# Kernel tuning notes

Hardware: AMD Instinct MI355X
Metric: run time of the kernel (lower is better)

## Reference

```python
import jax, jax.numpy as jnp
import numpy as np

B, S, D, H = 2, 2048, 1024, 16
DK = D // H

def setup_inputs() -> dict:
    key = jax.random.key(0)
    ks = jax.random.split(key, 11)
    def lin(kw, kb):
        # torch nn.Linear init scale ~ 1/sqrt(fan_in)
        s = 1.0 / np.sqrt(D)
        W = jax.random.uniform(kw, (D, D), jnp.float32, -s, s)
        b = jax.random.uniform(kb, (D,), jnp.float32, -s, s)
        return W, b
    Wq, bq = lin(ks[0], ks[1])
    Wk, bk = lin(ks[2], ks[3])
    Wv, bv = lin(ks[4], ks[5])
    Wo, bo = lin(ks[6], ks[7])
    query = jax.random.normal(ks[8], (B, S, D), jnp.float32)
    key_t = jax.random.normal(ks[9], (B, S, D), jnp.float32)
    value = jax.random.normal(ks[10], (B, S, D), jnp.float32)
    return {"query": query, "key": key_t, "value": value,
            "Wq": Wq, "bq": bq, "Wk": Wk, "bk": bk,
            "Wv": Wv, "bv": bv, "Wo": Wo, "bo": bo}

def reference(query, key, value, Wq, bq, Wk, bk, Wv, bv, Wo, bo):
    # linear projections (torch Linear: x @ W.T + b), split heads -> (B,H,S,DK)
    def proj(x, W, b):
        y = jnp.einsum('bsd,ed->bse', x, W) + b
        return y.reshape(B, -1, H, DK).transpose(0, 2, 1, 3)
    q = proj(query, Wq, bq)
    k = proj(key, Wk, bk)
    v = proj(value, Wv, bv)
    # scaled dot-product attention, full score matrix (B,H,Sq,Sk)
    scores = jnp.einsum('bhqd,bhkd->bhqk', q, k) / jnp.sqrt(jnp.float32(DK))
    attn = jax.nn.softmax(scores, axis=-1)
    ctx = jnp.einsum('bhqk,bhkd->bhqd', attn, v)
    # merge heads and output projection; dropout is identity in eval mode
    ctx = ctx.transpose(0, 2, 1, 3).reshape(B, -1, D)
    out = jnp.einsum('bsd,ed->bse', ctx, Wo) + bo
    attn_weights = attn.mean(axis=1)  # average_weights=True -> (B,Sq,Sk)
    return (out, attn_weights)
```

## Files before the change

### kernel.cpp

```cpp
#include <hip/hip_runtime.h>

#define B_ 2
#define S_ 2048
#define D_ 1024
#define H_ 16
#define DK_ 64
#define M_ (B_ * S_)

typedef __bf16 bf16;
typedef __attribute__((ext_vector_type(8))) __bf16 bf16x8;
typedef __attribute__((ext_vector_type(4))) __bf16 bf16x4;
typedef __attribute__((ext_vector_type(4))) float f32x4;

static __device__ __forceinline__ bf16x8 ld8(const bf16* p) {
    return *(const bf16x8*)p;
}

static __device__ __forceinline__ void g2l16(const void* g, void* l) {
    __builtin_amdgcn_global_load_lds(
        (const __attribute__((address_space(1))) unsigned int*)g,
        (__attribute__((address_space(3))) unsigned int*)l, 16, 0, 0);
}

__global__ __launch_bounds__(256)
void cvt_all(const float* __restrict__ xq, const float* __restrict__ xk,
             const float* __restrict__ xv, const float* __restrict__ wq,
             const float* __restrict__ wk, const float* __restrict__ wv,
             const float* __restrict__ wo, bf16* __restrict__ xqo,
             bf16* __restrict__ xko, bf16* __restrict__ xvo,
             bf16* __restrict__ wqo, bf16* __restrict__ wko,
             bf16* __restrict__ wvo, bf16* __restrict__ woo)
{
    const int bx = blockIdx.x;
    const float* s; bf16* d; size_t base;
    if (bx < 6144) {
        int a = bx >> 11;
        s = (a == 0) ? xq : (a == 1) ? xk : xv;
        d = (a == 0) ? xqo : (a == 1) ? xko : xvo;
        base = (size_t)(bx & 2047) * 2048;
    } else {
        int a = (bx - 6144) >> 9;
        s = (a == 0) ? wq : (a == 1) ? wk : (a == 2) ? wv : wo;
        d = (a == 0) ? wqo : (a == 1) ? wko : (a == 2) ? wvo : woo;
        base = (size_t)((bx - 6144) & 511) * 2048;
    }
    size_t i = base + (size_t)threadIdx.x * 8;
    f32x4 a4 = *(const f32x4*)(s + i);
    f32x4 b4 = *(const f32x4*)(s + i + 4);
    bf16x8 r;
    r[0]=(bf16)a4[0]; r[1]=(bf16)a4[1]; r[2]=(bf16)a4[2]; r[3]=(bf16)a4[3];
    r[4]=(bf16)b4[0]; r[5]=(bf16)b4[1]; r[6]=(bf16)b4[2]; r[7]=(bf16)b4[3];
    *(bf16x8*)(d + i) = r;
}

__global__ __launch_bounds__(256)
void gemm128(const bf16* __restrict__ A, const bf16* __restrict__ W,
             const float* __restrict__ bias, void* __restrict__ out,
             int a_headsplit, int out_mode, float scale)
{
    const int m0 = blockIdx.x * 128, n0 = blockIdx.y * 128;
    const int tid = threadIdx.x;
    const int wv = tid >> 6, lane = tid & 63, quad = lane >> 4, l16 = lane & 15;
    const int wr = (wv >> 1) * 64, wc = (wv & 1) * 64;

    __shared__ bf16 As[128 * 32];
    __shared__ bf16 Bs[128 * 32];

    f32x4 acc[4][4];
#pragma unroll
    for (int i = 0; i < 4; ++i)
#pragma unroll
        for (int j = 0; j < 4; ++j) acc[i][j] = f32x4{0.f, 0.f, 0.f, 0.f};

    const int srow = tid >> 2;
    const int scol = (tid & 3) * 8;

    for (int k0 = 0; k0 < D_; k0 += 32) {
        bf16x8 av[2], bw[2];
#pragma unroll
        for (int c = 0; c < 2; ++c) {
            const int row = c * 64 + srow;
            const int k   = k0 + scol;
            const bf16* ap;
            if (a_headsplit) {
                int m = m0 + row, bb = m >> 11, ss = m & (S_ - 1);
                int hh = k >> 6, dd = k & (DK_ - 1);
                ap = A + (((size_t)(bb * H_ + hh) * S_ + ss) * DK_ + dd);
            } else {
                ap = A + (size_t)(m0 + row) * D_ + k;
            }
            av[c] = ld8(ap);
            bw[c] = ld8(W + (size_t)(n0 + row) * D_ + k);
        }
        __syncthreads();
#pragma unroll
        for (int c = 0; c < 2; ++c) {
            const int e = c * 2048 + tid * 8;
            *(bf16x8*)(As + e) = av[c];
            *(bf16x8*)(Bs + e) = bw[c];
        }
        __syncthreads();

        bf16x8 af[4], bfr[4];
#pragma unroll
        for (int i = 0; i < 4; ++i)
            af[i] = *(const bf16x8*)(As + (wr + i*16 + l16) * 32 + quad * 8);
#pragma unroll
        for (int j = 0; j < 4; ++j)
            bfr[j] = *(const bf16x8*)(Bs + (wc + j*16 + l16) * 32 + quad * 8);
#pragma unroll
        for (int i = 0; i < 4; ++i)
#pragma unroll
            for (int j = 0; j < 4; ++j)
                acc[i][j] = __builtin_amdgcn_mfma_f32_16x16x32_bf16(
                    af[i], bfr[j], acc[i][j], 0, 0, 0);
    }

    if (out_mode == 2) {
#pragma unroll
        for (int j = 0; j < 4; ++j) {
            const int nn = n0 + wc + j*16 + l16;
            const float bvv = bias[nn];
            int hh = nn >> 6, dd = nn & (DK_ - 1);
#pragma unroll
            for (int ip = 0; ip < 2; ++ip) {
                const int mlo = m0 + wr + 32*ip + quad*4;
                int bb = mlo >> 11, sl = mlo & (S_ - 1);
                int g0 = (sl & ~31) + ((sl & 15) << 1);
                bf16x8 pk;
#pragma unroll
                for (int r = 0; r < 4; ++r) {
                    pk[2*r]   = (bf16)((acc[2*ip  ][j][r] + bvv) * scale);
                    pk[2*r+1] = (bf16)((acc[2*ip+1][j][r] + bvv) * scale);
                }
                *(bf16x8*)((bf16*)out +
                    ((size_t)(bb * H_ + hh) * DK_ + dd) * S_ + g0) = pk;
            }
        }
    } else {
#pragma unroll
        for (int i = 0; i < 4; ++i)
#pragma unroll
            for (int j = 0; j < 4; ++j) {
                const int nn = n0 + wc + j*16 + l16;
                const float bvv = bias[nn];
                const int mm0 = m0 + wr + i*16 + quad*4;
#pragma unroll
                for (int r = 0; r < 4; ++r) {
                    const int mm = mm0 + r;
                    float v = (acc[i][j][r] + bvv) * scale;
                    if (out_mode == 1) {
                        ((float*)out)[(size_t)mm * D_ + nn] = v;
                    } else {
                        int bb = mm >> 11, ss = mm & (S_ - 1);
                        int hh = nn >> 6, dd = nn & (DK_ - 1);
                        ((bf16*)out)[((size_t)(bb * H_ + hh) * S_ + ss) * DK_ + dd] = (bf16)v;
                    }
                }
            }
    }
}

__global__ __launch_bounds__(256)
void attn_ctx(const bf16* __restrict__ Q, const bf16* __restrict__ K,
              const bf16* __restrict__ Vt, float* __restrict__ Li,
              bf16* __restrict__ ctxOut)
{
    const int bid = blockIdx.x;
    const int l   = (bid & 7) * 128 + (bid >> 3);
    const int q0  = (l & 31) * 64;
    const int h   = (l >> 5) & 15;
    const int b   = l >> 9;

    const int tid = threadIdx.x;
    const int wv = tid >> 6, lane = tid & 63, quad = lane >> 4, l16 = lane & 15;

    __shared__ bf16 Kl[2][4096];
    __shared__ bf16 Vl[2][4096];

    const size_t hb = (size_t)(b * H_ + h) * S_;
    const int qw = q0 + wv * 16;

    bf16x8 qf0, qf1;
    {
        const bf16* qrow = Q + (hb + qw + l16) * DK_;
        qf0 = ld8(qrow + quad*8);
        qf1 = ld8(qrow + 32 + quad*8);
    }
    const char* Kbc = (const char*)(K  + hb * DK_);
    const char* Vbc = (const char*)(Vt + hb * DK_);

    f32x4 cacc[4];
#pragma unroll
    for (int db = 0; db < 4; ++db) cacc[db] = f32x4{0.f,0.f,0.f,0.f};
    float lsum = 0.f;

    const int rbK  = wv * 16;
    const int rlan = lane >> 3;
    const int off  = (((lane & 7) ^ rlan) << 4);

#define STAGE(jc, buf)                                                        \
    do {                                                                      \
        const size_t jb = (size_t)(jc) * 64;                                  \
        g2l16(Kbc + (jb + rbK + rlan) * 128 + off,      &Kl[buf][rbK*64]);    \
        g2l16(Kbc + (jb + rbK + 8 + rlan) * 128 + off,  &Kl[buf][(rbK+8)*64]);\
        g2l16(Vbc + (size_t)(rbK + rlan) * (S_*2) + jb*2 + off,               \
              &Vl[buf][rbK*64]);                                              \
        g2l16(Vbc + (size_t)(rbK + 8 + rlan) * (S_*2) + jb*2 + off,           \
              &Vl[buf][(rbK+8)*64]);                                          \
    } while (0)

    STAGE(0, 0);
    __syncthreads();

    int cur = 0;
    const int sw = (l16 & 7) << 4;
    for (int jc = 0; jc < 32; ++jc) {
        STAGE((jc + 1) & 31, cur ^ 1);

        const char* kb = (const char*)&Kl[cur][0];
        const char* vb = (const char*)&Vl[cur][0];

        f32x4 sc[4];
#pragma unroll
        for (int t = 0; t < 4; ++t) {
            const char* kr = kb + (t*16 + l16) * 128;
            bf16x8 ka = *(const bf16x8*)(kr + ((quad*16) ^ sw));
            bf16x8 kbv = *(const bf16x8*)(kr + ((64 + quad*16) ^ sw));
            f32x4 z = {0.f,0.f,0.f,0.f};
            z = __builtin_amdgcn_mfma_f32_16x16x32_bf16(ka, qf0, z, 0, 0, 0);
            sc[t] = __builtin_amdgcn_mfma_f32_16x16x32_bf16(kbv, qf1, z, 0, 0, 0);
        }

        float ex[4][4];
#pragma unroll
        for (int t = 0; t < 4; ++t)
#pragma unroll
            for (int r = 0; r < 4; ++r)
                ex[t][r] = __builtin_amdgcn_exp2f(fminf(sc[t][r], 86.f));
#pragma unroll
        for (int t = 0; t < 4; ++t)
            lsum += (ex[t][0] + ex[t][1]) + (ex[t][2] + ex[t][3]);

        bf16x8 pa0, pa1;
#pragma unroll
        for (int r = 0; r < 4; ++r) {
            pa0[2*r]   = (bf16)ex[0][r];
            pa0[2*r+1] = (bf16)ex[1][r];
            pa1[2*r]   = (bf16)ex[2][r];
            pa1[2*r+1] = (bf16)ex[3][r];
        }

#pragma unroll
        for (int db = 0; db < 4; ++db) {
            const char* vr = vb + (db*16 + l16) * 128;
            bf16x8 va0 = *(const bf16x8*)(vr + ((quad*16) ^ sw));
            bf16x8 va1 = *(const bf16x8*)(vr + ((64 + quad*16) ^ sw));
            cacc[db] = __builtin_amdgcn_mfma_f32_16x16x32_bf16(
                va0, pa0, cacc[db], 0, 0, 0);
            cacc[db] = __builtin_amdgcn_mfma_f32_16x16x32_bf16(
                va1, pa1, cacc[db], 0, 0, 0);
        }

        __syncthreads();
        cur ^= 1;
    }
#undef STAGE

    lsum += __shfl_xor(lsum, 16);
    lsum += __shfl_xor(lsum, 32);
    const float linv = 1.0f / fmaxf(lsum, 1e-30f);
    if (lane < 16) Li[hb + qw + lane] = lsum;

#pragma unroll
    for (int db = 0; db < 4; ++db) {
        bf16x4 pk;
#pragma unroll
        for (int r = 0; r < 4; ++r) pk[r] = (bf16)(cacc[db][r] * linv);
        *(bf16x4*)(ctxOut + (hb + qw + l16) * DK_ + db*16 + quad*4) = pk;
    }
}

__global__ __launch_bounds__(512)
void attn_weights(const bf16* __restrict__ Q, const bf16* __restrict__ K,
                  const float* __restrict__ Li, float* __restrict__ attnOut)
{
    const int bid = blockIdx.x;
    const int l   = (bid & 7) * 64 + (bid >> 3);
    const int q0  = (l & 31) * 64;
    const int b   = (l >> 5) & 1;
    const int j0  = (l >> 6) * 256;

    const int tid = threadIdx.x;
    const int wv = tid >> 6, lane = tid & 63, quad = lane >> 4, l16 = lane & 15;

    __shared__ float linv[H_][64];
    {
        int idx = tid * 2;
        int hh = idx >> 6, row = idx & 63;
        float v0 = (1.0f / H_) /
            fmaxf(Li[(size_t)(b * H_ + hh) * S_ + q0 + row], 1e-30f);
        float v1 = (1.0f / H_) /
            fmaxf(Li[(size_t)(b * H_ + hh) * S_ + q0 + row + 1], 1e-30f);
        linv[hh][row] = v0;
        linv[hh][row + 1] = v1;
    }
    __syncthreads();

    f32x4 asum[4][2];
#pragma unroll
    for (int qt = 0; qt < 4; ++qt)
#pragma unroll
        for (int t = 0; t < 2; ++t) asum[qt][t] = f32x4{0.f,0.f,0.f,0.f};

    for (int h = 0; h < H_; ++h) {
        const size_t hb = (size_t)(b * H_ + h) * S_;
        bf16x8 qf[4][2];
        float lv[4];
#pragma unroll
        for (int qt = 0; qt < 4; ++qt) {
            const bf16* qrow = Q + (hb + q0 + qt*16 + l16) * DK_;
            qf[qt][0] = ld8(qrow + quad*8);
            qf[qt][1] = ld8(qrow + 32 + quad*8);
            lv[qt] = linv[h][qt*16 + l16];
        }
        const bf16* Kb = K + hb * DK_;
#pragma unroll
        for (int t = 0; t < 2; ++t) {
            const int jl = j0 + wv*32 + t*16;
            const bf16* krow = Kb + (size_t)(jl + l16) * DK_;
            bf16x8 kfa = ld8(krow + quad*8), kfb = ld8(krow + 32 + quad*8);
#pragma unroll
            for (int qt = 0; qt < 4; ++qt) {
                f32x4 z = {0.f,0.f,0.f,0.f};
                z = __builtin_amdgcn_mfma_f32_16x16x32_bf16(kfa, qf[qt][0], z, 0, 0, 0);
                f32x4 s = __builtin_amdgcn_mfma_f32_16x16x32_bf16(kfb, qf[qt][1], z, 0, 0, 0);
#pragma unroll
                for (int r = 0; r < 4; ++r)
                    asum[qt][t][r] += __builtin_amdgcn_exp2f(fminf(s[r], 86.f)) * lv[qt];
            }
        }
    }
#pragma unroll
    for (int qt = 0; qt < 4; ++qt)
#pragma unroll
        for (int t = 0; t < 2; ++t)
            *(f32x4*)(attnOut + ((size_t)b * S_ + q0 + qt*16 + l16) * S_
                      + j0 + wv*32 + t*16 + quad*4) = asum[qt][t];
}

extern "C" void kernel_launch(void* const* d_in, const int* in_sizes, int n_in,
                              void* d_out, int out_size, void* d_ws, size_t ws_size,
                              hipStream_t stream)
{
    (void)in_sizes; (void)n_in; (void)out_size; (void)ws_size;

    const float* query = (const float*)d_in[0];
    const float* key_t = (const float*)d_in[1];
    const float* value = (const float*)d_in[2];
    const float* Wq = (const float*)d_in[3];
    const float* bq = (const float*)d_in[4];
    const float* Wk = (const float*)d_in[5];
    const float* bk = (const float*)d_in[6];
    const float* Wv = (const float*)d_in[7];
    const float* bv = (const float*)d_in[8];
    const float* Wo = (const float*)d_in[9];
    const float* bo = (const float*)d_in[10];

    float* out     = (float*)d_out;
    float* attnOut = out + (size_t)B_ * S_ * D_;

    const size_t nX = (size_t)B_ * S_ * D_;
    const size_t nW = (size_t)D_ * D_;

    bf16* Xqb = (bf16*)d_out;
    bf16* Xkb = Xqb + nX;
    bf16* Xvb = Xkb + nX;

    bf16* Qh  = (bf16*)d_ws;
    bf16* Kh  = Qh + nX;
    bf16* VtH = Kh + nX;
    bf16* Wob = VtH + nX;
    float* Li = (float*)(Wob + nW);
    bf16* Wqb = (bf16*)(Li + (size_t)B_ * H_ * S_);
    bf16* Wkb = Wqb + nW;
    bf16* Wvb = Wkb + nW;
    bf16* CtxH = Wqb;

    cvt_all<<<8192, 256, 0, stream>>>(query, key_t, value, Wq, Wk, Wv, Wo,
                                      Xqb, Xkb, Xvb, Wqb, Wkb, Wvb, Wob);
    dim3 gg(M_/128, D_/128);
    gemm128<<<gg, 256, 0, stream>>>(Xqb, Wqb, bq, Qh, 0, 0, 0.18033688011112042f);
    gemm128<<<gg, 256, 0, stream>>>(Xkb, Wkb, bk, Kh, 0, 0, 1.0f);
    gemm128<<<gg, 256, 0, stream>>>(Xvb, Wvb, bv, VtH, 0, 2, 1.0f);
    attn_ctx    <<<1024, 256, 0, stream>>>(Qh, Kh, VtH, Li, CtxH);
    attn_weights<<<512, 512, 0, stream>>>(Qh, Kh, Li, attnOut);
    gemm128<<<gg, 256, 0, stream>>>(CtxH, Wob, bo, out, 1, 1, 1.0f);
}
```

Baseline: 363.8 us.

## Double-buffer K tiles in LDS with async loads in attn_weights kernel

The attn_weights kernel now stages each head's 256-row K tile into LDS with global_load_lds, double-buffered so the next head's tile is fetched while the current one is used. An XOR swizzle on the 16-byte chunks is meant to avoid LDS bank conflicts when fragments are read back. The goal is to hide global-memory latency on K fragment loads behind the MFMA and exp work. In exchange the block uses 64KB of LDS, which can lower occupancy, and it adds a barrier per head. Each wave only reads rows it loaded itself, so there is no cross-wave reuse.

```diff
diff --git a/kernel.cpp b/kernel.cpp
--- a/kernel.cpp
+++ b/kernel.cpp
@@ -294,17 +294,30 @@
     const int tid = threadIdx.x;
     const int wv = tid >> 6, lane = tid & 63, quad = lane >> 4, l16 = lane & 15;
 
+    __shared__ bf16 Klds[2][256 * 64];
     __shared__ float linv[H_][64];
     {
         int idx = tid * 2;
         int hh = idx >> 6, row = idx & 63;
-        float v0 = (1.0f / H_) /
-            fmaxf(Li[(size_t)(b * H_ + hh) * S_ + q0 + row], 1e-30f);
-        float v1 = (1.0f / H_) /
-            fmaxf(Li[(size_t)(b * H_ + hh) * S_ + q0 + row + 1], 1e-30f);
-        linv[hh][row] = v0;
-        linv[hh][row + 1] = v1;
-    }
+        const float* Lp = Li + (size_t)(b * H_ + hh) * S_ + q0 + row;
+        linv[hh][row]     = (1.0f / H_) / fmaxf(Lp[0], 1e-30f);
+        linv[hh][row + 1] = (1.0f / H_) / fmaxf(Lp[1], 1e-30f);
+    }
+
+    const int rlan = lane >> 3;
+    const int off  = (((lane & 7) ^ rlan) << 4);
+    const char* Kbase = (const char*)(K + ((size_t)(b * H_) * S_ + j0) * DK_);
+
+#define WSTAGE(h, buf)                                                        \
+    do {                                                                      \
+        const char* src = Kbase + (size_t)(h) * (S_ * 128);                   \
+        for (int c = 0; c < 4; ++c) {                                         \
+            const int rr = wv * 32 + c * 8;                                   \
+            g2l16(src + (size_t)(rr + rlan) * 128 + off, &Klds[buf][rr * 64]);\
+        }                                                                     \
+    } while (0)
+
+    WSTAGE(0, 0);
     __syncthreads();
 
     f32x4 asum[4][2];
@@ -313,7 +326,11 @@
 #pragma unroll
         for (int t = 0; t < 2; ++t) asum[qt][t] = f32x4{0.f,0.f,0.f,0.f};
 
+    int cur = 0;
+    const int sw = (l16 & 7) << 4;
     for (int h = 0; h < H_; ++h) {
+        WSTAGE((h + 1) & 15, cur ^ 1);
+
         const size_t hb = (size_t)(b * H_ + h) * S_;
         bf16x8 qf[4][2];
         float lv[4];
@@ -324,12 +341,13 @@
             qf[qt][1] = ld8(qrow + 32 + quad*8);
             lv[qt] = linv[h][qt*16 + l16];
         }
-        const bf16* Kb = K + hb * DK_;
+
+        const char* kb = (const char*)&Klds[cur][0];
 #pragma unroll
         for (int t = 0; t < 2; ++t) {
-            const int jl = j0 + wv*32 + t*16;
-            const bf16* krow = Kb + (size_t)(jl + l16) * DK_;
-            bf16x8 kfa = ld8(krow + quad*8), kfb = ld8(krow + 32 + quad*8);
+            const char* kr = kb + (wv*32 + t*16 + l16) * 128;
+            bf16x8 kfa = *(const bf16x8*)(kr + ((quad*16) ^ sw));
+            bf16x8 kfb = *(const bf16x8*)(kr + ((64 + quad*16) ^ sw));
 #pragma unroll
             for (int qt = 0; qt < 4; ++qt) {
                 f32x4 z = {0.f,0.f,0.f,0.f};
@@ -340,7 +358,11 @@
                     asum[qt][t][r] += __builtin_amdgcn_exp2f(fminf(s[r], 86.f)) * lv[qt];
             }
         }
-    }
+        __syncthreads();
+        cur ^= 1;
+    }
+#undef WSTAGE
+
 #pragma unroll
     for (int qt = 0; qt < 4; ++qt)
 #pragma unroll
```

After: 354.9 us. -2.4%, faster.
